# Kernel tuning notes

Hardware: AMD Instinct MI355X
Metric: run time of the kernel (lower is better)

## Reference

```python
import jax, jax.numpy as jnp
import numpy as np

B, L, D, FF = 4, 4096, 1024, 2048
EPS = 1e-5


def _ln(x, g, b):
    m = jnp.mean(x, axis=-1, keepdims=True)
    v = jnp.var(x, axis=-1, keepdims=True)
    return (x - m) / jnp.sqrt(v + EPS) * g + b


def setup_inputs() -> dict:
    key = jax.random.key(0)
    ks = jax.random.split(key, 9)
    x = jax.random.normal(ks[0], (B, L, D), jnp.float32)
    # phazor init: exp(2j*pi*k/D) * |randn| -> split into re/im float params
    mag = jnp.abs(jax.random.normal(ks[1], (D,), jnp.float32))
    ang = 2.0 * jnp.pi * jnp.arange(D, dtype=jnp.float32) / D
    return dict(
        x=x,
        ln_g=jnp.ones((D,), jnp.float32),
        ln_b=jnp.zeros((D,), jnp.float32),
        fc_w=jax.random.normal(ks[2], (D, D), jnp.float32) * 0.02,
        fc_b=jnp.zeros((D,), jnp.float32),
        w1=jax.random.normal(ks[3], (D, FF), jnp.float32) * 0.02,
        b1=jnp.zeros((FF,), jnp.float32),
        w2=jax.random.normal(ks[4], (FF, D), jnp.float32) * 0.02,
        b2=jnp.zeros((D,), jnp.float32),
        ph_re=mag * jnp.cos(ang),
        ph_im=mag * jnp.sin(ang),
        phi_re=jax.random.normal(ks[5], (D,), jnp.float32),
        phi_im=jax.random.normal(ks[6], (D,), jnp.float32),
        lci_re=jax.random.normal(ks[7], (D,), jnp.float32),
        lci_im=jax.random.normal(ks[8], (D,), jnp.float32),
    )


def _spiral_conv(xn, ph_re, ph_im, phi_re, phi_im, lci_re, lci_im):
    ph = ph_re + 1j * ph_im          # phazor parameter [D]
    phi = phi_re + 1j * phi_im       # phazor_init [D]
    lci = lci_re + 1j * lci_im       # last_conv_init [D]
    a = jnp.abs(ph)
    phz = ph / a * jnp.exp(-a)       # unit direction * decaying magnitude, [D]
    t = jnp.arange(L, dtype=jnp.float32)[:, None]
    prog = jnp.exp(t * jnp.log(phz)[None, :])        # phz**t, [L, D]
    filt = prog * phi[None, :]                       # [L, D]
    filt_fft = jnp.fft.fft(filt, n=2 * L, axis=0)    # [2L, D]
    x_fft = jnp.fft.fft(xn.astype(jnp.complex64), n=2 * L, axis=1)  # [B, 2L, D]
    conv = jnp.fft.ifft(filt_fft[None] * x_fft, axis=1)[:, :L]      # [B, L, D]
    # last_conv is detached in the original (first call uses last_conv_init)
    last = jax.lax.stop_gradient(lci)
    conv = conv + last[None, None, :] * prog[None] * phz[None, None, :]
    return conv.real


def reference(x, ln_g, ln_b, fc_w, fc_b, w1, b1, w2, b2,
              ph_re, ph_im, phi_re, phi_im, lci_re, lci_im):
    xn = _ln(x, ln_g, ln_b)
    c = _spiral_conv(xn, ph_re, ph_im, phi_re, phi_im, lci_re, lci_im)
    y = jax.nn.silu(x @ fc_w + fc_b)
    x2 = c * y + x                  # gated conv + residual (dropout=0 -> identity)
    x3 = _ln(x2, ln_g, ln_b)        # same (shared) LayerNorm instance
    h = jax.nn.silu(x3 @ w1 + b1) @ w2 + b2
    return x2 + h
```

## Files before the change

kernel.cpp:

```cpp
#include <hip/hip_runtime.h>
#include <hip/hip_bf16.h>
#include <hip/hip_fp8.h>
#include <cstdint>
#include <cstddef>

#define B_ 4
#define L_ 4096
#define D_ 1024
#define FF_ 2048
#define ROWS (B_ * L_)
#define EPS_ 1e-5f
#define CG 64
#define CC 64

typedef __attribute__((ext_vector_type(8))) __bf16 bf16x8;
typedef __attribute__((ext_vector_type(4))) float f32x4;
typedef __attribute__((ext_vector_type(4))) unsigned short us4;

__device__ __forceinline__ float bf2f(unsigned short u) {
  union { unsigned int i; float f; } v; v.i = ((unsigned int)u) << 16; return v.f;
}
__device__ __forceinline__ unsigned short f2bf(float f) {
  union { float f; unsigned int i; } v; v.f = f;
  unsigned int r = v.i + 0x7fffu + ((v.i >> 16) & 1u);
  return (unsigned short)(r >> 16);
}
__device__ __forceinline__ unsigned char f2fp8(float f) {
  __hip_fp8_e4m3 q(f);
  return *reinterpret_cast<unsigned char*>(&q);
}

__global__ __launch_bounds__(256) void transpose_cast(
    const float* __restrict__ in, unsigned short* __restrict__ out, int K, int N) {
  __shared__ float tb[32][33];
  int n0 = blockIdx.x * 32, k0 = blockIdx.y * 32;
  int tx = threadIdx.x & 31, ty = threadIdx.x >> 5;
#pragma unroll
  for (int i = 0; i < 4; ++i) {
    int k = ty + i * 8;
    tb[k][tx] = in[(size_t)(k0 + k) * N + n0 + tx];
  }
  __syncthreads();
#pragma unroll
  for (int i = 0; i < 4; ++i) {
    int n = ty + i * 8;
    out[(size_t)(n0 + n) * K + k0 + tx] = f2bf(tb[tx][n]);
  }
}

__global__ __launch_bounds__(256) void transpose_cast_fp8(
    const float* __restrict__ in, unsigned char* __restrict__ out, int K, int N,
    float scale) {
  __shared__ float tb[32][33];
  int n0 = blockIdx.x * 32, k0 = blockIdx.y * 32;
  int tx = threadIdx.x & 31, ty = threadIdx.x >> 5;
#pragma unroll
  for (int i = 0; i < 4; ++i) {
    int k = ty + i * 8;
    tb[k][tx] = in[(size_t)(k0 + k) * N + n0 + tx];
  }
  __syncthreads();
#pragma unroll
  for (int i = 0; i < 4; ++i) {
    int n = ty + i * 8;
    out[(size_t)(n0 + n) * K + k0 + tx] = f2fp8(tb[tx][n] * scale);
  }
}

__global__ __launch_bounds__(256) void ln1_kernel(
    const float* __restrict__ x, const float* __restrict__ g, const float* __restrict__ b,
    unsigned short* __restrict__ xn, unsigned short* __restrict__ xb) {
  int row = blockIdx.x;
  int t = threadIdx.x;
  const float4* xr = (const float4*)(x + (size_t)row * D_);
  float4 v = xr[t];
  float s = v.x + v.y + v.z + v.w;
  float sq = v.x * v.x + v.y * v.y + v.z * v.z + v.w * v.w;
#pragma unroll
  for (int off = 32; off > 0; off >>= 1) {
    s += __shfl_down(s, off);
    sq += __shfl_down(sq, off);
  }
  __shared__ float ls[4], lq[4];
  int lane = t & 63, w = t >> 6;
  if (lane == 0) { ls[w] = s; lq[w] = sq; }
  __syncthreads();
  s = ls[0] + ls[1] + ls[2] + ls[3];
  sq = lq[0] + lq[1] + lq[2] + lq[3];
  float mean = s * (1.0f / D_);
  float var = sq * (1.0f / D_) - mean * mean;
  float rstd = rsqrtf(var + EPS_);
  float4 gv = ((const float4*)g)[t];
  float4 bv = ((const float4*)b)[t];
  us4 o, ob;
  o.x = f2bf((v.x - mean) * rstd * gv.x + bv.x);
  o.y = f2bf((v.y - mean) * rstd * gv.y + bv.y);
  o.z = f2bf((v.z - mean) * rstd * gv.z + bv.z);
  o.w = f2bf((v.w - mean) * rstd * gv.w + bv.w);
  ob.x = f2bf(v.x); ob.y = f2bf(v.y); ob.z = f2bf(v.z); ob.w = f2bf(v.w);
  ((us4*)(xn + (size_t)row * D_))[t] = o;
  ((us4*)(xb + (size_t)row * D_))[t] = ob;
}

__global__ __launch_bounds__(256) void conv_pass1(
    const unsigned short* __restrict__ xn, const float* __restrict__ ph_re,
    const float* __restrict__ ph_im, float2* __restrict__ rloc) {
  int d = blockIdx.x * 256 + threadIdx.x;
  int g = blockIdx.y, b = blockIdx.z;
  float re = ph_re[d], im = ph_im[d];
  float a = sqrtf(re * re + im * im);
  float sc = expf(-a) / a;
  float pr = re * sc, pi = im * sc;
  float rr = 0.f, ri = 0.f;
  const unsigned short* xp = xn + ((size_t)(b * L_ + g * CC)) * D_ + d;
#pragma unroll 8
  for (int l = 0; l < CC; ++l) {
    float xv = bf2f(xp[(size_t)l * D_]);
    float nr = pr * rr - pi * ri + xv;
    ri = pr * ri + pi * rr;
    rr = nr;
  }
  rloc[((size_t)(b * CG + g)) * D_ + d] = make_float2(rr, ri);
}

__global__ __launch_bounds__(256) void conv_pass2(
    const float* __restrict__ ph_re, const float* __restrict__ ph_im,
    const float2* __restrict__ rloc, float2* __restrict__ carry) {
  int idx = blockIdx.x * 256 + threadIdx.x;
  int b = idx >> 10, d = idx & (D_ - 1);
  float re = ph_re[d], im = ph_im[d];
  float a = sqrtf(re * re + im * im);
  float th = atan2f(im, re);
  float rho = expf(-a * (float)CC);
  float ang = th * (float)CC;
  float pcr = rho * cosf(ang), pci = rho * sinf(ang);
  float cr = 0.f, ci = 0.f;
  for (int g0 = 0; g0 < CG; g0 += 8) {
    float2 rl[8];
    float2 cw[8];
#pragma unroll
    for (int i = 0; i < 8; ++i)
      rl[i] = rloc[((size_t)(b * CG + g0 + i)) * D_ + d];
#pragma unroll
    for (int i = 0; i < 8; ++i) {
      cw[i] = make_float2(cr, ci);
      float nr = pcr * cr - pci * ci + rl[i].x;
      ci = pcr * ci + pci * cr + rl[i].y;
      cr = nr;
    }
#pragma unroll
    for (int i = 0; i < 8; ++i)
      carry[((size_t)(b * CG + g0 + i)) * D_ + d] = cw[i];
  }
}

__global__ __launch_bounds__(256) void conv_pass3(
    const unsigned short* __restrict__ xn,
    const float* __restrict__ ph_re, const float* __restrict__ ph_im,
    const float* __restrict__ phi_re, const float* __restrict__ phi_im,
    const float* __restrict__ lci_re, const float* __restrict__ lci_im,
    const float2* __restrict__ carry, unsigned short* __restrict__ cout) {
  int d = blockIdx.x * 256 + threadIdx.x;
  int g = blockIdx.y, b = blockIdx.z;
  float re = ph_re[d], im = ph_im[d];
  float a = sqrtf(re * re + im * im);
  float sc = expf(-a) / a;
  float pr = re * sc, pi = im * sc;
  float th = atan2f(im, re);
  int l0 = g * CC;
  float rho = expf(-a * (float)(l0 + 1));
  float ang = th * (float)(l0 + 1);
  float prr = rho * cosf(ang), pri = rho * sinf(ang);
  float fr = phi_re[d], fi = phi_im[d];
  float qr = lci_re[d], qi = lci_im[d];
  float2 cv = carry[((size_t)(b * CG + g)) * D_ + d];
  float rr = cv.x, ri = cv.y;
  const unsigned short* xp = xn + ((size_t)(b * L_ + l0)) * D_ + d;
  unsigned short* cp = cout + ((size_t)(b * L_ + l0)) * D_ + d;
#pragma unroll 4
  for (int l = 0; l < CC; ++l) {
    float xv = bf2f(xp[(size_t)l * D_]);
    float nr = pr * rr - pi * ri + xv;
    ri = pr * ri + pi * rr;
    rr = nr;
    float outv = fr * rr - fi * ri + qr * prr - qi * pri;
    cp[(size_t)l * D_] = f2bf(outv);
    float pn = pr * prr - pi * pri;
    pri = pr * pri + pi * prr;
    prr = pn;
  }
}

__global__ __launch_bounds__(256) void ln2c_kernel(
    const unsigned short* __restrict__ x2, const float* __restrict__ g,
    const float* __restrict__ b, unsigned char* __restrict__ x3) {
  int row = blockIdx.x;
  int t = threadIdx.x;
  size_t base = (size_t)row * D_;
  us4 vb = ((const us4*)(x2 + base))[t];
  float4 v;
  v.x = bf2f(vb.x); v.y = bf2f(vb.y); v.z = bf2f(vb.z); v.w = bf2f(vb.w);
  float s = v.x + v.y + v.z + v.w;
  float sq = v.x * v.x + v.y * v.y + v.z * v.z + v.w * v.w;
#pragma unroll
  for (int off = 32; off > 0; off >>= 1) {
    s += __shfl_down(s, off);
    sq += __shfl_down(sq, off);
  }
  __shared__ float ls[4], lq[4];
  int lane = t & 63, w = t >> 6;
  if (lane == 0) { ls[w] = s; lq[w] = sq; }
  __syncthreads();
  s = ls[0] + ls[1] + ls[2] + ls[3];
  sq = lq[0] + lq[1] + lq[2] + lq[3];
  float mean = s * (1.0f / D_);
  float var = sq * (1.0f / D_) - mean * mean;
  float rstd = rsqrtf(var + EPS_);
  float4 gv = ((const float4*)g)[t];
  float4 bv = ((const float4*)b)[t];
  uchar4 o;
  o.x = f2fp8((v.x - mean) * rstd * gv.x + bv.x);
  o.y = f2fp8((v.y - mean) * rstd * gv.y + bv.y);
  o.z = f2fp8((v.z - mean) * rstd * gv.z + bv.z);
  o.w = f2fp8((v.w - mean) * rstd * gv.w + bv.w);
  ((uchar4*)(x3 + base))[t] = o;
}

__device__ __forceinline__ void gld_lds16(const void* gp, void* lp) {
  __builtin_amdgcn_global_load_lds(
      (const __attribute__((address_space(1))) unsigned int*)gp,
      (__attribute__((address_space(3))) unsigned int*)lp, 16, 0, 0);
}

#define PHASE_SYNC()                                         \
  __builtin_amdgcn_s_barrier();                              \
  asm volatile("s_waitcnt lgkmcnt(0)" ::: "memory");         \
  __builtin_amdgcn_sched_barrier(0);                         \
  __builtin_amdgcn_s_setprio(1);

#define PHASE_END()                                          \
  __builtin_amdgcn_s_setprio(0);

template <int SILU, int OUT_BF16, int GATE>
__global__ __launch_bounds__(512) void gemm_bt(
    const unsigned short* __restrict__ A, const unsigned short* __restrict__ Bt,
    const float* __restrict__ bias,
    const unsigned short* __restrict__ gate, const unsigned short* __restrict__ xresb,
    void* __restrict__ Cv, int NB, int GROUP, int N, int K) {
  __shared__ unsigned short As[3][256 * 64];
  __shared__ unsigned short Bs[3][128 * 64];

  int nwg = gridDim.x;
  int xcd = blockIdx.x & 7;
  int lo = blockIdx.x >> 3;
  int q = nwg >> 3;
  int gsz = GROUP * NB;
  int g_ = lo / gsz, r_ = lo % gsz;
  int n_ = r_ / GROUP, ml = r_ - n_ * GROUP;
  int Mx = q / NB;
  int bm0 = (xcd * Mx + g_ * GROUP + ml) * 256;
  int bn0 = n_ * 128;

  int t = threadIdx.x;
  int lane = t & 63, w = t >> 6;
  int wr = w >> 1, wc = w & 1;
  int frr = lane & 15, cl = lane >> 4;
  int fx = frr & 7;
  int rA0 = wr * 64 + frr;
  int rB0 = wc * 64 + frr;
  int ko0 = (cl ^ fx) * 8;
  int ko1 = ((4 + cl) ^ fx) * 8;

  int nt = K >> 6;

  int tr = t >> 3;
  int jx = (t & 7) ^ (tr & 7);
  const unsigned short* pA = A + (size_t)(bm0 + tr) * K + jx * 8;
  const unsigned short* pB = Bt + (size_t)(bn0 + tr) * K + jx * 8;

  auto stA = [&](int kt2, int slot, int c) {
    gld_lds16(pA + (size_t)kt2 * 64 + (size_t)c * 64 * K, &As[slot][c * 4096 + t * 8]);
  };
  auto stB = [&](int kt2, int slot, int c) {
    gld_lds16(pB + (size_t)kt2 * 64 + (size_t)c * 64 * K, &Bs[slot][c * 4096 + t * 8]);
  };

  f32x4 acc[4][4] = {};

  stA(0, 0, 0); stA(0, 0, 1); stA(0, 0, 2); stA(0, 0, 3); stB(0, 0, 0); stB(0, 0, 1);
  stA(1, 1, 0); stA(1, 1, 1); stA(1, 1, 2); stA(1, 1, 3); stB(1, 1, 0); stB(1, 1, 1);
  asm volatile("s_waitcnt vmcnt(6)" ::: "memory");
  __builtin_amdgcn_s_barrier();

  int s = 0;
  for (int kt = 0; kt < nt; ++kt) {
    const unsigned short* as = As[s];
    const unsigned short* bs = Bs[s];
    int s2 = s + 2; if (s2 >= 3) s2 -= 3;
    bool p2 = kt + 2 < nt;

    bf16x8 a0[4], b0[4];
#pragma unroll
    for (int m = 0; m < 4; ++m) a0[m] = *(const bf16x8*)&as[(rA0 + m * 16) * 64 + ko0];
#pragma unroll
    for (int n = 0; n < 4; ++n) b0[n] = *(const bf16x8*)&bs[(rB0 + n * 16) * 64 + ko0];
    if (p2) { stA(kt + 2, s2, 0); stA(kt + 2, s2, 1); stB(kt + 2, s2, 0); }
    PHASE_SYNC();
#pragma unroll
    for (int m = 0; m < 4; ++m)
#pragma unroll
      for (int n = 0; n < 4; ++n)
        acc[m][n] = __builtin_amdgcn_mfma_f32_16x16x32_bf16(a0[m], b0[n], acc[m][n], 0, 0, 0);
    PHASE_END();
    __builtin_amdgcn_s_barrier();

    bf16x8 a1[4], b1[4];
#pragma unroll
    for (int m = 0; m < 4; ++m) a1[m] = *(const bf16x8*)&as[(rA0 + m * 16) * 64 + ko1];
#pragma unroll
    for (int n = 0; n < 4; ++n) b1[n] = *(const bf16x8*)&bs[(rB0 + n * 16) * 64 + ko1];
    if (p2) { stA(kt + 2, s2, 2); stA(kt + 2, s2, 3); stB(kt + 2, s2, 1); }
    PHASE_SYNC();
#pragma unroll
    for (int m = 0; m < 4; ++m)
#pragma unroll
      for (int n = 0; n < 4; ++n)
        acc[m][n] = __builtin_amdgcn_mfma_f32_16x16x32_bf16(a1[m], b1[n], acc[m][n], 0, 0, 0);
    PHASE_END();
    if (p2) { asm volatile("s_waitcnt vmcnt(6)" ::: "memory"); }
    else    { asm volatile("s_waitcnt vmcnt(0)" ::: "memory"); }
    __builtin_amdgcn_s_barrier();
    s += 1; if (s == 3) s = 0;
  }

#pragma unroll
  for (int m = 0; m < 4; ++m) {
#pragma unroll
    for (int n = 0; n < 4; ++n) {
#pragma unroll
      for (int r = 0; r < 4; ++r) {
        int row = bm0 + wr * 64 + m * 16 + cl * 4 + r;
        int col = bn0 + wc * 64 + n * 16 + frr;
        size_t o = (size_t)row * N + col;
        float v = acc[m][n][r] + bias[col];
        if (SILU) v = v / (1.0f + __expf(-v));
        if (GATE) v = bf2f(gate[o]) * v + bf2f(xresb[o]);
        if (OUT_BF16)
          ((unsigned short*)Cv)[o] = f2bf(v);
        else
          ((float*)Cv)[o] = v;
      }
    }
  }
}

template <int SILU, int RESBF, int OUT_FP8>
__global__ __launch_bounds__(512, 4) void gemm_f8(
    const unsigned char* __restrict__ A, const unsigned char* __restrict__ Bt,
    const float* __restrict__ bias, const unsigned short* __restrict__ resb,
    float oscale, void* __restrict__ Cv, int NB, int GROUP, int N, int K) {
  __shared__ unsigned char As[3][256 * 64];
  __shared__ unsigned char Bs[3][128 * 64];

  int nwg = gridDim.x;
  int xcd = blockIdx.x & 7;
  int lo = blockIdx.x >> 3;
  int q = nwg >> 3;
  int gsz = GROUP * NB;
  int g_ = lo / gsz, r_ = lo % gsz;
  int n_ = r_ / GROUP, ml = r_ - n_ * GROUP;
  int Mx = q / NB;
  int bm0 = (xcd * Mx + g_ * GROUP + ml) * 256;
  int bn0 = n_ * 128;

  int t = threadIdx.x;
  int lane = t & 63, w = t >> 6;
  int wr = w >> 1, wc = w & 1;
  int frr = lane & 15, cl = lane >> 4;
  int sw = (frr >> 1) & 3;
  int rA0 = wr * 64 + frr;
  int rB0 = wc * 64 + frr;
  int ko0 = ((((cl >> 1) ^ sw) << 4) | ((cl & 1) << 3));
  int ko1 = (((((cl >> 1) + 2) ^ sw) << 4) | ((cl & 1) << 3));

  int nt = K >> 6;

  int tr = t >> 2;
  int jc = (t & 3) ^ ((tr >> 1) & 3);
  const unsigned char* pA = A + (size_t)(bm0 + tr) * K + jc * 16;
  const unsigned char* pB = Bt + (size_t)(bn0 + tr) * K + jc * 16;

  auto stA = [&](int kt2, int slot, int c) {
    gld_lds16(pA + (size_t)kt2 * 64 + (size_t)c * 128 * K, &As[slot][c * 8192 + t * 16]);
  };
  auto stB = [&](int kt2, int slot) {
    gld_lds16(pB + (size_t)kt2 * 64, &Bs[slot][t * 16]);
  };

  f32x4 acc[4][4] = {};

  stA(0, 0, 0); stA(0, 0, 1); stB(0, 0);
  stA(1, 1, 0); stA(1, 1, 1); stB(1, 1);
  asm volatile("s_waitcnt vmcnt(3)" ::: "memory");
  __builtin_amdgcn_s_barrier();

  int s = 0;
  for (int kt = 0; kt < nt; ++kt) {
    const unsigned char* as = As[s];
    const unsigned char* bs = Bs[s];
    int s2 = s + 2; if (s2 >= 3) s2 -= 3;
    bool p2 = kt + 2 < nt;

    long a0[4], b0[4];
#pragma unroll
    for (int m = 0; m < 4; ++m) a0[m] = *(const long*)&as[(rA0 + m * 16) * 64 + ko0];
#pragma unroll
    for (int n = 0; n < 4; ++n) b0[n] = *(const long*)&bs[(rB0 + n * 16) * 64 + ko0];
    if (p2) { stA(kt + 2, s2, 0); stA(kt + 2, s2, 1); }
    PHASE_SYNC();
#pragma unroll
    for (int m = 0; m < 4; ++m)
#pragma unroll
      for (int n = 0; n < 4; ++n)
        acc[m][n] = __builtin_amdgcn_mfma_f32_16x16x32_fp8_fp8(a0[m], b0[n], acc[m][n], 0, 0, 0);
    PHASE_END();
    __builtin_amdgcn_s_barrier();

    long a1[4], b1[4];
#pragma unroll
    for (int m = 0; m < 4; ++m) a1[m] = *(const long*)&as[(rA0 + m * 16) * 64 + ko1];
#pragma unroll
    for (int n = 0; n < 4; ++n) b1[n] = *(const long*)&bs[(rB0 + n * 16) * 64 + ko1];
    if (p2) stB(kt + 2, s2);
    PHASE_SYNC();
#pragma unroll
    for (int m = 0; m < 4; ++m)
#pragma unroll
      for (int n = 0; n < 4; ++n)
        acc[m][n] = __builtin_amdgcn_mfma_f32_16x16x32_fp8_fp8(a1[m], b1[n], acc[m][n], 0, 0, 0);
    PHASE_END();
    if (p2) { asm volatile("s_waitcnt vmcnt(3)" ::: "memory"); }
    else    { asm volatile("s_waitcnt vmcnt(0)" ::: "memory"); }
    __builtin_amdgcn_s_barrier();
    s += 1; if (s == 3) s = 0;
  }

#pragma unroll
  for (int m = 0; m < 4; ++m) {
#pragma unroll
    for (int n = 0; n < 4; ++n) {
#pragma unroll
      for (int r = 0; r < 4; ++r) {
        int row = bm0 + wr * 64 + m * 16 + cl * 4 + r;
        int col = bn0 + wc * 64 + n * 16 + frr;
        size_t o = (size_t)row * N + col;
        float v = acc[m][n][r] * oscale + bias[col];
        if (SILU) v = v / (1.0f + __expf(-v));
        if (RESBF) v += bf2f(resb[o]);
        if (OUT_FP8)
          ((unsigned char*)Cv)[o] = f2fp8(v);
        else
          ((float*)Cv)[o] = v;
      }
    }
  }
}

extern "C" void kernel_launch(void* const* d_in, const int* in_sizes, int n_in,
                              void* d_out, int out_size, void* d_ws, size_t ws_size,
                              hipStream_t stream) {
  const float* x      = (const float*)d_in[0];
  const float* ln_g   = (const float*)d_in[1];
  const float* ln_b   = (const float*)d_in[2];
  const float* fc_w   = (const float*)d_in[3];
  const float* fc_b   = (const float*)d_in[4];
  const float* w1     = (const float*)d_in[5];
  const float* b1     = (const float*)d_in[6];
  const float* w2     = (const float*)d_in[7];
  const float* b2     = (const float*)d_in[8];
  const float* ph_re  = (const float*)d_in[9];
  const float* ph_im  = (const float*)d_in[10];
  const float* phi_re = (const float*)d_in[11];
  const float* phi_im = (const float*)d_in[12];
  const float* lci_re = (const float*)d_in[13];
  const float* lci_im = (const float*)d_in[14];
  float* out = (float*)d_out;

  char* ws = (char*)d_ws;
  const size_t SZ_BF = (size_t)ROWS * D_ * 2;
  const size_t SZ_F8 = (size_t)ROWS * D_;
  unsigned short* xn_x2 = (unsigned short*)(ws);
  unsigned short* cbuf  = (unsigned short*)(ws + SZ_BF);
  unsigned short* xb    = (unsigned short*)(ws + 2 * SZ_BF);
  unsigned char*  x3f8  = (unsigned char*)(ws + 3 * SZ_BF);
  unsigned char*  h1f8  = (unsigned char*)(ws + 3 * SZ_BF + SZ_F8);
  char* wp = ws + 3 * SZ_BF + SZ_F8 + (size_t)ROWS * FF_;
  unsigned short* fc_wt = (unsigned short*)(wp);
  unsigned char*  w1t8  = (unsigned char*)(wp + (size_t)D_ * D_ * 2);
  unsigned char*  w2t8  = (unsigned char*)(wp + (size_t)D_ * D_ * 2 + (size_t)D_ * FF_);
  float2* rloc  = (float2*)(wp + (size_t)D_ * D_ * 2 + 2 * (size_t)D_ * FF_);
  float2* carry = rloc + (size_t)B_ * CG * D_;

  transpose_cast<<<dim3(D_ / 32, D_ / 32), 256, 0, stream>>>(fc_w, fc_wt, D_, D_);
  transpose_cast_fp8<<<dim3(FF_ / 32, D_ / 32), 256, 0, stream>>>(w1, w1t8, D_, FF_, 32.0f);
  transpose_cast_fp8<<<dim3(D_ / 32, FF_ / 32), 256, 0, stream>>>(w2, w2t8, FF_, D_, 32.0f);

  ln1_kernel<<<ROWS, 256, 0, stream>>>(x, ln_g, ln_b, xn_x2, xb);

  conv_pass1<<<dim3(D_ / 256, CG, B_), 256, 0, stream>>>(xn_x2, ph_re, ph_im, rloc);
  conv_pass2<<<dim3((B_ * D_) / 256), 256, 0, stream>>>(ph_re, ph_im, rloc, carry);
  conv_pass3<<<dim3(D_ / 256, CG, B_), 256, 0, stream>>>(xn_x2, ph_re, ph_im, phi_re, phi_im,
                                                         lci_re, lci_im, carry, cbuf);

  gemm_bt<1, 1, 1><<<(ROWS / 256) * (D_ / 128), 512, 0, stream>>>(
      xb, fc_wt, fc_b, cbuf, xb, xn_x2, D_ / 128, 4, D_, D_);

  ln2c_kernel<<<ROWS, 256, 0, stream>>>(xn_x2, ln_g, ln_b, x3f8);

  gemm_f8<1, 0, 1><<<(ROWS / 256) * (FF_ / 128), 512, 0, stream>>>(
      x3f8, w1t8, b1, nullptr, 1.0f / 32.0f, h1f8, FF_ / 128, 4, FF_, D_);

  gemm_f8<0, 1, 0><<<(ROWS / 256) * (D_ / 128), 512, 0, stream>>>(
      h1f8, w2t8, b2, xn_x2, 1.0f / 32.0f, out, D_ / 128, 2, D_, FF_);
}
```

Baseline: 261.6 us.

## Merge fp8 GEMM k-phases into one barrier per tile, use fp32 residual

In the fp8 GEMM loop, both k-halves of the LDS fragments are now read up front, and all next-tile prefetches (A and B) are issued together. The two MFMA phases then run back to back with a single barrier per k-tile instead of three. This lowers barrier overhead but keeps more fragment registers live, which may affect occupancy at launch bounds of 4 waves. Separately, the gated fc GEMM is de-templated and now adds the fp32 x residual instead of a bf16 copy, which improves accuracy but reads twice as many residual bytes.

```diff
diff --git a/kernel.cpp b/kernel.cpp
--- a/kernel.cpp
+++ b/kernel.cpp
@@ -241,12 +241,11 @@
 #define PHASE_END()                                          \
   __builtin_amdgcn_s_setprio(0);
 
-template <int SILU, int OUT_BF16, int GATE>
-__global__ __launch_bounds__(512) void gemm_bt(
+__global__ __launch_bounds__(512) void gemm_bt_gate(
     const unsigned short* __restrict__ A, const unsigned short* __restrict__ Bt,
     const float* __restrict__ bias,
-    const unsigned short* __restrict__ gate, const unsigned short* __restrict__ xresb,
-    void* __restrict__ Cv, int NB, int GROUP, int N, int K) {
+    const unsigned short* __restrict__ gate, const float* __restrict__ xresf,
+    unsigned short* __restrict__ Cv, int NB, int GROUP, int N, int K) {
   __shared__ unsigned short As[3][256 * 64];
   __shared__ unsigned short Bs[3][128 * 64];
 
@@ -343,12 +342,9 @@
         int col = bn0 + wc * 64 + n * 16 + frr;
         size_t o = (size_t)row * N + col;
         float v = acc[m][n][r] + bias[col];
-        if (SILU) v = v / (1.0f + __expf(-v));
-        if (GATE) v = bf2f(gate[o]) * v + bf2f(xresb[o]);
-        if (OUT_BF16)
-          ((unsigned short*)Cv)[o] = f2bf(v);
-        else
-          ((float*)Cv)[o] = v;
+        v = v / (1.0f + __expf(-v));
+        v = bf2f(gate[o]) * v + xresf[o];
+        Cv[o] = f2bf(v);
       }
     }
   }
@@ -411,34 +407,32 @@
     int s2 = s + 2; if (s2 >= 3) s2 -= 3;
     bool p2 = kt + 2 < nt;
 
-    long a0[4], b0[4];
+    long a0[4], b0[4], a1[4], b1[4];
 #pragma unroll
     for (int m = 0; m < 4; ++m) a0[m] = *(const long*)&as[(rA0 + m * 16) * 64 + ko0];
 #pragma unroll
     for (int n = 0; n < 4; ++n) b0[n] = *(const long*)&bs[(rB0 + n * 16) * 64 + ko0];
-    if (p2) { stA(kt + 2, s2, 0); stA(kt + 2, s2, 1); }
-    PHASE_SYNC();
+#pragma unroll
+    for (int m = 0; m < 4; ++m) a1[m] = *(const long*)&as[(rA0 + m * 16) * 64 + ko1];
+#pragma unroll
+    for (int n = 0; n < 4; ++n) b1[n] = *(const long*)&bs[(rB0 + n * 16) * 64 + ko1];
+    if (p2) { stA(kt + 2, s2, 0); stA(kt + 2, s2, 1); stB(kt + 2, s2); }
+
+    asm volatile("s_waitcnt lgkmcnt(0)" ::: "memory");
+    __builtin_amdgcn_sched_barrier(0);
+    __builtin_amdgcn_s_setprio(1);
 #pragma unroll
     for (int m = 0; m < 4; ++m)
 #pragma unroll
       for (int n = 0; n < 4; ++n)
         acc[m][n] = __builtin_amdgcn_mfma_f32_16x16x32_fp8_fp8(a0[m], b0[n], acc[m][n], 0, 0, 0);
-    PHASE_END();
-    __builtin_amdgcn_s_barrier();
-
-    long a1[4], b1[4];
-#pragma unroll
-    for (int m = 0; m < 4; ++m) a1[m] = *(const long*)&as[(rA0 + m * 16) * 64 + ko1];
-#pragma unroll
-    for (int n = 0; n < 4; ++n) b1[n] = *(const long*)&bs[(rB0 + n * 16) * 64 + ko1];
-    if (p2) stB(kt + 2, s2);
-    PHASE_SYNC();
 #pragma unroll
     for (int m = 0; m < 4; ++m)
 #pragma unroll
       for (int n = 0; n < 4; ++n)
         acc[m][n] = __builtin_amdgcn_mfma_f32_16x16x32_fp8_fp8(a1[m], b1[n], acc[m][n], 0, 0, 0);
-    PHASE_END();
+    __builtin_amdgcn_s_setprio(0);
+
     if (p2) { asm volatile("s_waitcnt vmcnt(3)" ::: "memory"); }
     else    { asm volatile("s_waitcnt vmcnt(0)" ::: "memory"); }
     __builtin_amdgcn_s_barrier();
@@ -512,8 +506,8 @@
   conv_pass3<<<dim3(D_ / 256, CG, B_), 256, 0, stream>>>(xn_x2, ph_re, ph_im, phi_re, phi_im,
                                                          lci_re, lci_im, carry, cbuf);
 
-  gemm_bt<1, 1, 1><<<(ROWS / 256) * (D_ / 128), 512, 0, stream>>>(
-      xb, fc_wt, fc_b, cbuf, xb, xn_x2, D_ / 128, 4, D_, D_);
+  gemm_bt_gate<<<(ROWS / 256) * (D_ / 128), 512, 0, stream>>>(
+      xb, fc_wt, fc_b, cbuf, x, xn_x2, D_ / 128, 4, D_, D_);
 
   ln2c_kernel<<<ROWS, 256, 0, stream>>>(xn_x2, ln_g, ln_b, x3f8);
 
```

New measurement: 269.5 us. +3.0%, slower.
